# Kernel tuning notes

Measured on AMD Instinct MI355X. Metric: run time of the kernel, lower is better.

Reference implementation:

```python
import jax, jax.numpy as jnp
import numpy as np

HEADS = 8
DIM_HEAD = 128
EPS = 1e-5


def layer_norm(t, gamma):
    mu = jnp.mean(t, axis=-1, keepdims=True)
    var = jnp.var(t, axis=-1, keepdims=True)
    return (t - mu) / jnp.sqrt(var + EPS) * gamma


def setup_inputs() -> dict:
    key = jax.random.key(0)
    k1, k2, k3 = jax.random.split(key, 3)
    B, N, T, D = 16, 256, 4096, 1024
    img_queries = jax.random.normal(k1, (B, N, D), dtype=jnp.float32)
    x = jax.random.normal(k2, (B, T, D), dtype=jnp.float32)
    gamma_q = jnp.ones((D,), dtype=jnp.float32)
    gamma_x = jnp.ones((D,), dtype=jnp.float32)
    W_kv = jax.random.normal(k3, (D, 2 * DIM_HEAD), dtype=jnp.float32) * 0.02
    return {"img_queries": img_queries, "x": x, "gamma_q": gamma_q,
            "gamma_x": gamma_x, "W_kv": W_kv}


def reference(img_queries, x, gamma_q, gamma_x, W_kv):
    B, N, D = img_queries.shape
    scale = DIM_HEAD ** -0.5
    q_n = layer_norm(img_queries, gamma_q)            # [B,N,D]
    x_n = layer_norm(x, gamma_x)                      # [B,T,D]
    # b n (h d) -> b h n d
    q = q_n.reshape(B, N, HEADS, DIM_HEAD).transpose(0, 2, 1, 3)
    kv = x_n @ W_kv                                   # [B,T,2*dim_head]
    k = kv[..., :DIM_HEAD]                            # shared single K head; v chunk unused
    sim = jnp.einsum('bhid,bjd->bhij', q * scale, k)  # [B,H,N,T]
    sim = sim - jnp.max(sim, axis=-1, keepdims=True)
    attn = jax.nn.softmax(sim, axis=-1)
    out = jnp.einsum('bhij,bjf->bhif', attn, x_n)     # V = raw normed x, [B,H,N,D]
    # b h n f -> b (n h f)
    out = out.transpose(0, 2, 1, 3).reshape(B, N * HEADS * D)
    return out, attn
```

## Files before the change

### kernel.cpp

```cpp
#include <hip/hip_runtime.h>

typedef unsigned short u16;
typedef unsigned int u32;
typedef __attribute__((ext_vector_type(8))) short short8;
typedef __attribute__((ext_vector_type(4))) float f32x4;
typedef __attribute__((ext_vector_type(4))) unsigned int u32x4;

#define SCALE 0.08838834764831845f
#define OUT_ELEMS 33554432ull

__device__ __forceinline__ u16 f2b(float f) {
  u32 u = __float_as_uint(f);
  u32 r = u + 0x7fffu + ((u >> 16) & 1u);
  return (u16)(r >> 16);
}

__device__ __forceinline__ u32 cvtpk(float lo, float hi) {
  u32 r;
  asm("v_cvt_pk_bf16_f32 %0, %1, %2" : "=v"(r) : "v"(lo), "v"(hi));
  return r;
}

__device__ __forceinline__ void gload16(const void* g, void* l) {
  __builtin_amdgcn_global_load_lds((const __attribute__((address_space(1))) void*)g,
                                   (__attribute__((address_space(3))) void*)l, 16, 0, 0);
}

__device__ __forceinline__ uint2 shflx2(uint2 v, int m) {
  uint2 r;
  r.x = __shfl_xor(v.x, m, 64);
  r.y = __shfl_xor(v.y, m, 64);
  return r;
}

__global__ __launch_bounds__(256) void ln_rows(const float* __restrict__ in,
                                               const float* __restrict__ gamma,
                                               u16* __restrict__ out, float scale) {
  const int row = blockIdx.x;
  const int t = threadIdx.x;
  const float4 v = *(const float4*)(in + (size_t)row * 1024 + t * 4);
  float s = v.x + v.y + v.z + v.w;
  float q = v.x * v.x + v.y * v.y + v.z * v.z + v.w * v.w;
#pragma unroll
  for (int m = 32; m; m >>= 1) {
    s += __shfl_down(s, m);
    q += __shfl_down(q, m);
  }
  __shared__ float red[8];
  const int w = t >> 6;
  if ((t & 63) == 0) { red[w] = s; red[4 + w] = q; }
  __syncthreads();
  s = red[0] + red[1] + red[2] + red[3];
  q = red[4] + red[5] + red[6] + red[7];
  const float mu = s * (1.0f / 1024.0f);
  const float var = q * (1.0f / 1024.0f) - mu * mu;
  const float rs = rsqrtf(var + 1e-5f) * scale;
  const float4 g = *(const float4*)(gamma + t * 4);
  ushort4 o;
  o.x = f2b((v.x - mu) * rs * g.x);
  o.y = f2b((v.y - mu) * rs * g.y);
  o.z = f2b((v.z - mu) * rs * g.z);
  o.w = f2b((v.w - mu) * rs * g.w);
  *(ushort4*)(out + (size_t)row * 1024 + t * 4) = o;
}

__global__ __launch_bounds__(1024) void ln_xpose(const float* __restrict__ in,
                                                 const float* __restrict__ gamma,
                                                 u16* __restrict__ xn,
                                                 u16* __restrict__ xnt) {
  __shared__ u16 tile[32][1024];
  const int blk = blockIdx.x;
  const int b = blk >> 7;
  const int jj0 = (blk & 127) * 32;
  const int t = threadIdx.x;
  const int lane = t & 63, w = t >> 6;
  const size_t j0 = (size_t)blk * 32;

  float4 gv[4];
#pragma unroll
  for (int k = 0; k < 4; ++k) gv[k] = *(const float4*)(gamma + k * 256 + lane * 4);

  float4 va[2][4];
  float mu[2], rs[2];
#pragma unroll
  for (int rr = 0; rr < 2; ++rr) {
    const int row = w * 2 + rr;
    const float* src = in + (j0 + row) * 1024;
    float s = 0.f, q = 0.f;
#pragma unroll
    for (int k = 0; k < 4; ++k) {
      const float4 v = *(const float4*)(src + k * 256 + lane * 4);
      va[rr][k] = v;
      s += v.x + v.y + v.z + v.w;
      q += v.x * v.x + v.y * v.y + v.z * v.z + v.w * v.w;
    }
#pragma unroll
    for (int m = 1; m < 64; m <<= 1) {
      s += __shfl_xor(s, m);
      q += __shfl_xor(q, m);
    }
    const float m_ = s * (1.0f / 1024.0f);
    mu[rr] = m_;
    rs[rr] = rsqrtf(q * (1.0f / 1024.0f) - m_ * m_ + 1e-5f);
  }
#pragma unroll
  for (int rr = 0; rr < 2; ++rr) {
    const int row = w * 2 + rr;
    u16* xrow = xn + (j0 + row) * 1024;
#pragma unroll
    for (int k = 0; k < 4; ++k) {
      const float4 v = va[rr][k];
      uint2 p;
      p.x = cvtpk((v.x - mu[rr]) * rs[rr] * gv[k].x, (v.y - mu[rr]) * rs[rr] * gv[k].y);
      p.y = cvtpk((v.z - mu[rr]) * rs[rr] * gv[k].z, (v.w - mu[rr]) * rs[rr] * gv[k].w);
      *(uint2*)(xrow + k * 256 + lane * 4) = p;
      *(uint2*)(&tile[row][k * 256 + lane * 4]) = p;
    }
  }
  __syncthreads();
  u32 o[16];
#pragma unroll
  for (int r = 0; r < 16; ++r)
    o[r] = (u32)tile[2 * r][t] | ((u32)tile[2 * r + 1][t] << 16);
  u16* dst = xnt + ((size_t)b * 1024 + t) * 4096 + jj0;
#pragma unroll
  for (int k = 0; k < 4; ++k) {
    u32x4 v = {o[4 * k + 0], o[4 * k + 1], o[4 * k + 2], o[4 * k + 3]};
    *(u32x4*)(dst + k * 8) = v;
  }
}

__global__ __launch_bounds__(256) void cvt_w(const float* __restrict__ w, u16* __restrict__ wt) {
  const int n = blockIdx.x;
  const int t = threadIdx.x;
  const int d = t * 4;
  ushort4 o;
  o.x = f2b(w[(size_t)(d + 0) * 256 + n]);
  o.y = f2b(w[(size_t)(d + 1) * 256 + n]);
  o.z = f2b(w[(size_t)(d + 2) * 256 + n]);
  o.w = f2b(w[(size_t)(d + 3) * 256 + n]);
  *(ushort4*)(wt + (size_t)n * 1024 + d) = o;
}

__global__ __launch_bounds__(256) void kgemm(const u16* __restrict__ xn,
                                             const u16* __restrict__ wt,
                                             u16* __restrict__ ks) {
  __shared__ u16 As[128 * 32];
  __shared__ u16 Bs[128 * 32];
  const int t = threadIdx.x;
  const int lane = t & 63, w = t >> 6;
  const int wm = w >> 1, wn = w & 1;
  const int j0 = blockIdx.x * 128;
  const int g = lane >> 4, r16 = lane & 15;
  f32x4 acc[4][4] = {};
  for (int k0 = 0; k0 < 1024; k0 += 32) {
    __syncthreads();
#pragma unroll
    for (int i = 0; i < 2; ++i) {
      const int seg = i * 4 + w;
      const int off = seg * 1024 + lane * 16;
      const int row = off >> 6;
      const int c = (off >> 4) & 3;
      const int sw = c ^ ((row >> 1) & 3);
      gload16(xn + ((size_t)(j0 + row)) * 1024 + k0 + sw * 8, (char*)As + seg * 1024);
      gload16(wt + ((size_t)row) * 1024 + k0 + sw * 8, (char*)Bs + seg * 1024);
    }
    __syncthreads();
    short8 a[4], bq[4];
#pragma unroll
    for (int mt = 0; mt < 4; ++mt) {
      const int row = wm * 64 + mt * 16 + r16;
      const int sw = g ^ ((row >> 1) & 3);
      a[mt] = *(const short8*)(As + row * 32 + sw * 8);
    }
#pragma unroll
    for (int nt = 0; nt < 4; ++nt) {
      const int row = wn * 64 + nt * 16 + r16;
      const int sw = g ^ ((row >> 1) & 3);
      bq[nt] = *(const short8*)(Bs + row * 32 + sw * 8);
    }
#pragma unroll
    for (int mt = 0; mt < 4; ++mt)
#pragma unroll
      for (int nt = 0; nt < 4; ++nt)
        acc[mt][nt] = __builtin_amdgcn_mfma_f32_16x16x32_bf16(a[mt], bq[nt], acc[mt][nt], 0, 0, 0);
  }
#pragma unroll
  for (int mt = 0; mt < 4; ++mt)
#pragma unroll
    for (int nt = 0; nt < 4; ++nt)
#pragma unroll
      for (int r = 0; r < 4; ++r) {
        const int j = j0 + wm * 64 + mt * 16 + g * 4 + r;
        const int n = wn * 64 + nt * 16 + r16;
        ks[(size_t)j * 128 + n] = f2b(acc[mt][nt][r]);
      }
}

__global__ __launch_bounds__(1024, 1) void attn_kernel(const u16* __restrict__ qs,
                                                       const u16* __restrict__ ks,
                                                       u16* __restrict__ attnb) {
  const int orig = blockIdx.x;
  const int blk = (orig & 7) * 256 + (orig >> 3);
  const int it = blk & 15, h = (blk >> 4) & 7, b = blk >> 7;
  const int i0 = it * 16;
  const int t = threadIdx.x;
  const int lane = t & 63, w = t >> 6;
  const int g = lane >> 4, r16 = lane & 15;
  __shared__ u16 Q[16 * 128];
  __shared__ float redm[256];
  __shared__ float reds[256];
  if (t < 256) {
    const int row = t >> 4, c = t & 15;
    const int sw = c ^ (row & 7);
    *(short8*)(Q + row * 128 + sw * 8) =
        *(const short8*)(qs + ((size_t)(b * 256 + i0 + row)) * 1024 + h * 128 + c * 8);
  }
  __syncthreads();
  short8 a[4];
#pragma unroll
  for (int kp = 0; kp < 4; ++kp) {
    const int c = kp * 4 + g;
    const int sw = c ^ (r16 & 7);
    a[kp] = *(const short8*)(Q + r16 * 128 + sw * 8);
  }
  const u16* kb = ks + (size_t)b * 4096 * 128;
  const int j0 = w * 256;
  f32x4 acc[16] = {};
#pragma unroll
  for (int kp = 0; kp < 4; ++kp) {
    short8 bv[16];
#pragma unroll
    for (int nt = 0; nt < 16; ++nt)
      bv[nt] = *(const short8*)(kb + (size_t)(j0 + nt * 16 + r16) * 128 + kp * 32 + g * 8);
#pragma unroll
    for (int nt = 0; nt < 16; ++nt)
      acc[nt] = __builtin_amdgcn_mfma_f32_16x16x32_bf16(bv[nt], a[kp], acc[nt], 0, 0, 0);
  }
  float mx = acc[0][0];
#pragma unroll
  for (int nt = 0; nt < 16; ++nt)
#pragma unroll
    for (int r = 0; r < 4; ++r) mx = fmaxf(mx, acc[nt][r]);
  mx = fmaxf(mx, __shfl_xor(mx, 16));
  mx = fmaxf(mx, __shfl_xor(mx, 32));
  float sm = 0.f;
#pragma unroll
  for (int nt = 0; nt < 16; ++nt)
#pragma unroll
    for (int r = 0; r < 4; ++r) {
      const float p = __expf(acc[nt][r] - mx);
      acc[nt][r] = p;
      sm += p;
    }
  sm += __shfl_xor(sm, 16);
  sm += __shfl_xor(sm, 32);
  if (lane < 16) {
    redm[w * 16 + lane] = mx;
    reds[w * 16 + lane] = sm;
  }
  __syncthreads();
  float m = redm[r16];
#pragma unroll
  for (int w2 = 1; w2 < 16; ++w2) m = fmaxf(m, redm[w2 * 16 + r16]);
  float s = 0.f;
#pragma unroll
  for (int w2 = 0; w2 < 16; ++w2)
    s += reds[w2 * 16 + r16] * __expf(redm[w2 * 16 + r16] - m);
  const float f = __expf(mx - m) / s;
#pragma unroll
  for (int nt = 0; nt < 16; ++nt) acc[nt] *= f;

  u16* brow = attnb + ((size_t)((b * 8 + h) * 256 + i0 + r16)) * 4096 + j0;
  const bool gb0 = (g & 1), gb1 = (g & 2);
#pragma unroll
  for (int q4 = 0; q4 < 4; ++q4) {
    uint2 X[4];
#pragma unroll
    for (int i = 0; i < 4; ++i) {
      const f32x4 v = acc[q4 * 4 + i];
      X[i] = make_uint2(cvtpk(v[0], v[1]), cvtpk(v[2], v[3]));
    }
#pragma unroll
    for (int k = 0; k < 2; ++k) {
      const uint2 aa = X[2 * k], bb = X[2 * k + 1];
      const uint2 sent = gb0 ? aa : bb;
      const uint2 recv = shflx2(sent, 16);
      X[2 * k] = gb0 ? recv : aa;
      X[2 * k + 1] = gb0 ? bb : recv;
    }
#pragma unroll
    for (int k = 0; k < 2; ++k) {
      const uint2 aa = X[k], bb = X[k + 2];
      const uint2 sent = gb1 ? aa : bb;
      const uint2 recv = shflx2(sent, 32);
      X[k] = gb1 ? recv : aa;
      X[k + 2] = gb1 ? bb : recv;
    }
    u16* bp = brow + q4 * 64 + g * 16;
    u32x4 o0 = {X[0].x, X[0].y, X[1].x, X[1].y};
    u32x4 o1 = {X[2].x, X[2].y, X[3].x, X[3].y};
    *(u32x4*)bp = o0;
    *(u32x4*)(bp + 8) = o1;
  }
}

__global__ __launch_bounds__(512, 2) void ogemm256(const u16* __restrict__ attnb,
                                                   const u16* __restrict__ xnt,
                                                   float* __restrict__ out,
                                                   float* __restrict__ attn) {
  extern __shared__ u16 S[];
  const int orig = blockIdx.x;
  const int wid = (orig & 7) * 64 + (orig >> 3);
  const int b = wid >> 5, ft = (wid >> 3) & 3, h = wid & 7;
  const int t = threadIdx.x;
  const int lane = t & 63, w = t >> 6;
  const int wm = w >> 2, wn = w & 3;
  const int g = lane >> 4, r16 = lane & 15;
  const u16* Ab = attnb + ((size_t)(b * 8 + h) * 256) * 4096;
  const u16* Bb = xnt + ((size_t)b * 1024 + ft * 256) * 4096;
  const int wrow = ft * 64 + (t >> 3);
  const int wci = t & 7;
  float* wdst = attn + ((size_t)(b * 8 + h) * 256 + wrow) * 4096 + wci * 8;

  int srow[4], scol[4];
#pragma unroll
  for (int seg = 0; seg < 4; ++seg) {
    const int gi = seg * 512 + t;
    srow[seg] = gi >> 3;
    scol[seg] = (((gi & 7) ^ ((gi >> 3) & 7)) * 8);
  }
  const int wuni = w * 1024;

#define OSTAGE(buf, k0)                                                         \
  do {                                                                          \
    _Pragma("unroll") for (int seg = 0; seg < 4; ++seg)                         \
        gload16(Ab + (size_t)srow[seg] * 4096 + (k0) + scol[seg],               \
                (char*)S + (buf)*32768 + seg * 8192 + wuni);                    \
    _Pragma("unroll") for (int seg = 0; seg < 4; ++seg)                         \
        gload16(Bb + (size_t)srow[seg] * 4096 + (k0) + scol[seg],               \
                (char*)S + 65536 + (buf)*32768 + seg * 8192 + wuni);            \
  } while (0)

  f32x4 acc[8][4] = {};
  OSTAGE(0, 0);
  OSTAGE(1, 64);
  asm volatile("s_waitcnt vmcnt(8)" ::: "memory");
  __builtin_amdgcn_s_barrier();

  for (int t64 = 0; t64 < 64; ++t64) {
    const int buf = t64 & 1;
    const char* A0 = (const char*)S + buf * 32768;
    const char* B0 = (const char*)S + 65536 + buf * 32768;
    short8 af[8], bf[4];
#pragma unroll
    for (int mt = 0; mt < 8; ++mt) {
      const int row = wm * 128 + mt * 16 + r16;
      af[mt] = *(const short8*)(A0 + row * 128 + ((g ^ (row & 7)) * 16));
    }
#pragma unroll
    for (int nt = 0; nt < 4; ++nt) {
      const int row = wn * 64 + nt * 16 + r16;
      bf[nt] = *(const short8*)(B0 + row * 128 + ((g ^ (row & 7)) * 16));
    }
    asm volatile("s_waitcnt lgkmcnt(0)" ::: "memory");
    __builtin_amdgcn_sched_barrier(0);
    __builtin_amdgcn_s_setprio(1);
#pragma unroll
    for (int mt = 0; mt < 8; ++mt)
#pragma unroll
      for (int nt = 0; nt < 4; ++nt)
        acc[mt][nt] = __builtin_amdgcn_mfma_f32_16x16x32_bf16(af[mt], bf[nt], acc[mt][nt], 0, 0, 0);
    __builtin_amdgcn_s_setprio(0);
#pragma unroll
    for (int mt = 0; mt < 8; ++mt) {
      const int row = wm * 128 + mt * 16 + r16;
      af[mt] = *(const short8*)(A0 + row * 128 + (((4 + g) ^ (row & 7)) * 16));
    }
#pragma unroll
    for (int nt = 0; nt < 4; ++nt) {
      const int row = wn * 64 + nt * 16 + r16;
      bf[nt] = *(const short8*)(B0 + row * 128 + (((4 + g) ^ (row & 7)) * 16));
    }
    const short8 wv = *(const short8*)(A0 + wrow * 128 + ((wci ^ (wrow & 7)) * 16));
    asm volatile("s_waitcnt lgkmcnt(0)" ::: "memory");
    __builtin_amdgcn_sched_barrier(0);
    {
      f32x4 lo, hi;
#pragma unroll
      for (int e = 0; e < 4; ++e) {
        lo[e] = __uint_as_float(((u32)(u16)wv[e]) << 16);
        hi[e] = __uint_as_float(((u32)(u16)wv[4 + e]) << 16);
      }
      float* dst = wdst + t64 * 64;
      __builtin_nontemporal_store(lo, (f32x4*)dst);
      __builtin_nontemporal_store(hi, (f32x4*)(dst + 4));
      __builtin_amdgcn_sched_barrier(0);
    }
    __builtin_amdgcn_s_barrier();
    if (t64 + 2 < 64) OSTAGE(buf, (t64 + 2) * 64);
    __builtin_amdgcn_s_setprio(1);
#pragma unroll
    for (int mt = 0; mt < 8; ++mt)
#pragma unroll
      for (int nt = 0; nt < 4; ++nt)
        acc[mt][nt] = __builtin_amdgcn_mfma_f32_16x16x32_bf16(af[mt], bf[nt], acc[mt][nt], 0, 0, 0);
    __builtin_amdgcn_s_setprio(0);
    if (t64 + 2 < 64) {
      asm volatile("s_waitcnt vmcnt(10)" ::: "memory");
    } else if (t64 == 62) {
      asm volatile("s_waitcnt vmcnt(0)" ::: "memory");
    }
    __builtin_amdgcn_s_barrier();
  }
#undef OSTAGE

  float* ob = out + (size_t)b * 2097152 + (size_t)h * 1024;
#pragma unroll
  for (int mt = 0; mt < 8; ++mt)
#pragma unroll
    for (int nt = 0; nt < 4; ++nt)
#pragma unroll
      for (int r = 0; r < 4; ++r) {
        const int i = wm * 128 + mt * 16 + g * 4 + r;
        const int f = ft * 256 + wn * 64 + nt * 16 + r16;
        ob[(size_t)i * 8192 + f] = acc[mt][nt][r];
      }
}

extern "C" void kernel_launch(void* const* d_in, const int* in_sizes, int n_in,
                              void* d_out, int out_size, void* d_ws, size_t ws_size,
                              hipStream_t stream) {
  const float* img_q = (const float*)d_in[0];
  const float* x = (const float*)d_in[1];
  const float* gamma_q = (const float*)d_in[2];
  const float* gamma_x = (const float*)d_in[3];
  const float* wkv = (const float*)d_in[4];

  float* out_f = (float*)d_out;
  float* attn_f = out_f + OUT_ELEMS;

  u16* xn = (u16*)attn_f;
  u16* qsb = (u16*)out_f;
  u16* wtb = qsb + 4194304;
  u16* ksb = wtb + 131072;
  u16* xnt = (u16*)d_ws;
  u16* attnb = xnt + 67108864;

  if (ws_size < (size_t)402653184) return;

  (void)hipFuncSetAttribute((const void*)ogemm256,
                            hipFuncAttributeMaxDynamicSharedMemorySize, 131072);

  ln_xpose<<<2048, 1024, 0, stream>>>(x, gamma_x, xn, xnt);
  ln_rows<<<4096, 256, 0, stream>>>(img_q, gamma_q, qsb, SCALE);
  cvt_w<<<128, 256, 0, stream>>>(wkv, wtb);
  kgemm<<<512, 256, 0, stream>>>(xn, wtb, ksb);
  attn_kernel<<<2048, 1024, 0, stream>>>(qsb, ksb, attnb);
  ogemm256<<<512, 512, 131072, stream>>>(attnb, xnt, out_f, attn_f);
}
```

Before: 810.8 us.

## Stage K tiles through LDS with double-buffered async loads in attn_kernel

The attention score kernel used to load all K fragments for each k-slice straight from global memory into registers. It now streams 64-row K tiles into a per-wave double-buffered LDS region with global_load_lds and a swizzled layout, waiting on vmcnt so the next tile's load overlaps the current MFMAs. This needs 128KB of dynamic shared memory per block and adds explicit waitcnt and sched barriers. It lowers register pressure from the 16 short8 fragments, but the overlap is limited because each stage feeds only 4 MFMAs.

After: 713.1 us. 12.1% less time.

```diff
diff --git a/kernel.cpp b/kernel.cpp
--- a/kernel.cpp
+++ b/kernel.cpp
@@ -200,13 +200,14 @@
 __global__ __launch_bounds__(1024, 1) void attn_kernel(const u16* __restrict__ qs,
                                                        const u16* __restrict__ ks,
                                                        u16* __restrict__ attnb) {
+  extern __shared__ char KS[];
   const int orig = blockIdx.x;
   const int blk = (orig & 7) * 256 + (orig >> 3);
   const int it = blk & 15, h = (blk >> 4) & 7, b = blk >> 7;
   const int i0 = it * 16;
   const int t = threadIdx.x;
   const int lane = t & 63, w = t >> 6;
-  const int g = lane >> 4, r16 = lane & 15;
+  const int gq = lane >> 4, r16 = lane & 15;
   __shared__ u16 Q[16 * 128];
   __shared__ float redm[256];
   __shared__ float reds[256];
@@ -220,23 +221,51 @@
   short8 a[4];
 #pragma unroll
   for (int kp = 0; kp < 4; ++kp) {
-    const int c = kp * 4 + g;
+    const int c = kp * 4 + gq;
     const int sw = c ^ (r16 & 7);
     a[kp] = *(const short8*)(Q + r16 * 128 + sw * 8);
   }
   const u16* kb = ks + (size_t)b * 4096 * 128;
   const int j0 = w * 256;
+  const int srow = lane >> 2;
+  const int scol = ((lane & 3) ^ (srow & 3)) * 8;
+  char* wbuf = KS + w * 8192;
+
+#define STAGEK(gg)                                                                \
+  do {                                                                            \
+    const int kp_ = (gg) >> 2, q_ = (gg)&3;                                       \
+    const u16* s0 = kb + (size_t)(j0 + q_ * 64 + srow) * 128 + kp_ * 32 + scol;   \
+    char* d0 = wbuf + ((gg)&1) * 4096;                                            \
+    gload16(s0, d0);                                                              \
+    gload16(s0 + 2048, d0 + 1024);                                                \
+    gload16(s0 + 4096, d0 + 2048);                                                \
+    gload16(s0 + 6144, d0 + 3072);                                                \
+  } while (0)
+
   f32x4 acc[16] = {};
-#pragma unroll
-  for (int kp = 0; kp < 4; ++kp) {
-    short8 bv[16];
-#pragma unroll
-    for (int nt = 0; nt < 16; ++nt)
-      bv[nt] = *(const short8*)(kb + (size_t)(j0 + nt * 16 + r16) * 128 + kp * 32 + g * 8);
-#pragma unroll
-    for (int nt = 0; nt < 16; ++nt)
-      acc[nt] = __builtin_amdgcn_mfma_f32_16x16x32_bf16(bv[nt], a[kp], acc[nt], 0, 0, 0);
-  }
+  STAGEK(0);
+  const int rb = r16 * 64 + ((gq ^ (r16 & 3)) * 16);
+#pragma unroll
+  for (int gg = 0; gg < 16; ++gg) {
+    if (gg + 1 < 16) STAGEK(gg + 1);
+    if (gg + 1 < 16)
+      asm volatile("s_waitcnt vmcnt(4)" ::: "memory");
+    else
+      asm volatile("s_waitcnt vmcnt(0)" ::: "memory");
+    __builtin_amdgcn_sched_barrier(0);
+    const char* buf = wbuf + (gg & 1) * 4096;
+    short8 bv[4];
+#pragma unroll
+    for (int i = 0; i < 4; ++i) bv[i] = *(const short8*)(buf + i * 1024 + rb);
+    asm volatile("s_waitcnt lgkmcnt(0)" ::: "memory");
+    __builtin_amdgcn_sched_barrier(0);
+    const int kp = gg >> 2, q = gg & 3;
+#pragma unroll
+    for (int i = 0; i < 4; ++i)
+      acc[q * 4 + i] = __builtin_amdgcn_mfma_f32_16x16x32_bf16(bv[i], a[kp], acc[q * 4 + i], 0, 0, 0);
+  }
+#undef STAGEK
+
   float mx = acc[0][0];
 #pragma unroll
   for (int nt = 0; nt < 16; ++nt)
@@ -272,7 +301,7 @@
   for (int nt = 0; nt < 16; ++nt) acc[nt] *= f;
 
   u16* brow = attnb + ((size_t)((b * 8 + h) * 256 + i0 + r16)) * 4096 + j0;
-  const bool gb0 = (g & 1), gb1 = (g & 2);
+  const bool gb0 = (gq & 1), gb1 = (gq & 2);
 #pragma unroll
   for (int q4 = 0; q4 < 4; ++q4) {
     uint2 X[4];
@@ -297,7 +326,7 @@
       X[k] = gb1 ? recv : aa;
       X[k + 2] = gb1 ? bb : recv;
     }
-    u16* bp = brow + q4 * 64 + g * 16;
+    u16* bp = brow + q4 * 64 + gq * 16;
     u32x4 o0 = {X[0].x, X[0].y, X[1].x, X[1].y};
     u32x4 o1 = {X[2].x, X[2].y, X[3].x, X[3].y};
     *(u32x4*)bp = o0;
@@ -451,11 +480,13 @@
 
   (void)hipFuncSetAttribute((const void*)ogemm256,
                             hipFuncAttributeMaxDynamicSharedMemorySize, 131072);
+  (void)hipFuncSetAttribute((const void*)attn_kernel,
+                            hipFuncAttributeMaxDynamicSharedMemorySize, 131072);
 
   ln_xpose<<<2048, 1024, 0, stream>>>(x, gamma_x, xn, xnt);
   ln_rows<<<4096, 256, 0, stream>>>(img_q, gamma_q, qsb, SCALE);
   cvt_w<<<128, 256, 0, stream>>>(wkv, wtb);
   kgemm<<<512, 256, 0, stream>>>(xn, wtb, ksb);
-  attn_kernel<<<2048, 1024, 0, stream>>>(qsb, ksb, attnb);
+  attn_kernel<<<2048, 1024, 131072, stream>>>(qsb, ksb, attnb);
   ogemm256<<<512, 512, 131072, stream>>>(attnb, xnt, out_f, attn_f);
 }
```
